# Optimization experiments

Hardware: AMD Instinct MI355X
Metric: run time of the kernel (lower is better)

Reference implementation:

```python
import jax, jax.numpy as jnp
import numpy as np

B, V, H, W, CIN, COUT = 2, 4, 256, 256, 64, 64
WINDOW = 1
GAMMA = 0.1


def setup_inputs() -> dict:
    key = jax.random.key(0)
    ks = jax.random.split(key, 6)
    # gaussian positions: x,y in [-1,1], z in [0.5,2.5] so projection masks are nontrivial
    means = jax.random.uniform(ks[0], (B, V, H, W, 3), dtype=jnp.float32)
    means = means * jnp.array([2.0, 2.0, 2.0], jnp.float32) + jnp.array([-1.0, -1.0, 0.5], jnp.float32)
    depths = jax.random.uniform(ks[1], (B, V, H, W, 1, 1), dtype=jnp.float32)
    gs_feats = jax.random.normal(ks[2], (B, V, H, W, CIN), dtype=jnp.float32)
    # normalized intrinsics (ndc in [0,1))
    intr = jnp.array([[0.8, 0.0, 0.5], [0.0, 0.8, 0.5], [0.0, 0.0, 1.0]], jnp.float32)
    intrinsics = jnp.broadcast_to(intr, (B, V, 3, 3))
    # camera-to-world extrinsics: identity rotation, small per-view translations
    t = jax.random.uniform(ks[3], (B, V, 3), minval=-0.2, maxval=0.2, dtype=jnp.float32)
    extrinsics = jnp.broadcast_to(jnp.eye(4, dtype=jnp.float32), (B, V, 4, 4)).at[..., :3, 3].set(t)
    w1 = jax.random.normal(ks[4], (COUT, CIN, 3, 3), dtype=jnp.float32) * 0.05
    b1 = jnp.zeros((COUT,), jnp.float32)
    w2 = jax.random.normal(ks[5], (COUT, COUT, 3, 3), dtype=jnp.float32) * 0.05
    b2 = jnp.zeros((COUT,), jnp.float32)
    return {"means": means, "depths": depths, "gs_feats": gs_feats,
            "intrinsics": intrinsics, "extrinsics": extrinsics,
            "w1": w1, "b1": b1, "w2": w2, "b2": b2}


def _project(points, intr, extr, eps=1e-8):
    # points (b, n, 3) world; extr (b,4,4) cam-to-world; intr (b,3,3) normalized
    w2c = jnp.linalg.inv(extr)
    ph = jnp.concatenate([points, jnp.ones_like(points[..., :1])], axis=-1)  # (b,n,4)
    cam = jnp.einsum('bij,bnj->bni', w2c, ph)[..., :3]
    z = cam[..., 2:3]
    ndc = jnp.einsum('bij,bnj->bni', intr, cam / (z + eps))
    return ndc[..., :2], cam[..., 2] > eps


def _conv3x3(x, w, b):
    y = jax.lax.conv_general_dilated(x, w, (1, 1), 'SAME',
                                     dimension_numbers=('NCHW', 'OIHW', 'NCHW'))
    return y + b[None, :, None, None]


def reference(means, depths, gs_feats, intrinsics, extrinsics, w1, b1, w2, b2):
    b, v, h, w_, c = gs_feats.shape
    hw = h * w_
    feats_flat = gs_feats.reshape(b, v, hw, c)
    pts = means.reshape(b, v, hw, 3)
    outs = []
    for j in range(v):
        acc = feats_flat[:, j]                      # (b, hw, c)
        norm = jnp.ones((b,), gs_feats.dtype)
        for k in range(v):
            if j != k and (k - WINDOW) <= j <= (k + WINDOW):
                ndc, valid_z = _project(pts[:, j], intrinsics[:, k], extrinsics[:, k])
                px = jnp.floor(ndc[..., 0] * w_).astype(jnp.int32)
                py = jnp.floor(ndc[..., 1] * h).astype(jnp.int32)
                mask = ((ndc[..., 0] >= 0) & (ndc[..., 0] < 1) &
                        (ndc[..., 1] >= 0) & (ndc[..., 1] < 1) & valid_z)  # (b,hw)
                idx = jnp.clip(py, 0, h - 1) * w_ + jnp.clip(px, 0, w_ - 1)
                gathered = jnp.take_along_axis(feats_flat[:, k], idx[..., None], axis=1)
                upd = jnp.where(mask[..., None], gathered, jnp.zeros((), gs_feats.dtype))
                scale = GAMMA * mask.sum(-1).astype(gs_feats.dtype) / (h * w_)  # (b,)
                acc = acc + upd * scale[:, None, None]
                norm = norm + scale
        outs.append(acc / norm[:, None, None])
    fused = jnp.stack(outs, axis=1).reshape(b * v, h, w_, c).transpose(0, 3, 1, 2)  # (bv,c,h,w)
    x = _conv3x3(fused, w1, b1)
    x = jax.nn.gelu(x, approximate=False)
    x = _conv3x3(x, w2, b2)
    return x.transpose(0, 2, 3, 1).reshape(b, v, h, w_, -1)
```

## Files before the change

### kernel.cpp

```cpp
#include <hip/hip_runtime.h>
#include <math.h>

#define HW 65536
#define NPAD 258

typedef short bf16x8 __attribute__((ext_vector_type(8)));
typedef float f32x4  __attribute__((ext_vector_type(4)));

#define O_COUNTS 0
#define O_W2C    2048
#define O_WT     4096
#define O_META   151552
#define O_FUSED  3297280
#define O_X1     71458816

#define HROWB   4224
#define HROWSTR 4240
#define HBUFB   (6 * HROWSTR)

__device__ __forceinline__ unsigned short f2bf(float f) {
    unsigned int u = __float_as_uint(f);
    u += 0x7FFFu + ((u >> 16) & 1u);
    return (unsigned short)(u >> 16);
}

__device__ __forceinline__ unsigned int cvt_pk_bf16(float lo, float hi) {
    unsigned int r;
    asm("v_cvt_pk_bf16_f32 %0, %1, %2" : "=v"(r) : "v"(lo), "v"(hi));
    return r;
}

__device__ __forceinline__ float gelu_fast(float v) {
    float x  = v * 0.70710678118654752f;
    float ax = fabsf(x);
    float t  = __builtin_amdgcn_rcpf(fmaf(0.3275911f, ax, 1.0f));
    float p  = fmaf(t, 1.061405429f, -1.453152027f);
    p = fmaf(t, p, 1.421413741f);
    p = fmaf(t, p, -0.284496736f);
    p = fmaf(t, p, 0.254829592f);
    p = p * t;
    float e   = __expf(-x * x);
    float era = fmaf(-p, e, 1.0f);
    float er  = copysignf(era, x);
    return 0.5f * v * (1.0f + er);
}

__global__ __launch_bounds__(256) void prep_kernel(
    const float* __restrict__ extr, const float* __restrict__ w1,
    const float* __restrict__ w2, float* __restrict__ w2c,
    unsigned short* __restrict__ wT, unsigned short* __restrict__ fusedP,
    unsigned short* __restrict__ x1P, int* __restrict__ counts)
{
    int tid = blockIdx.x * blockDim.x + threadIdx.x;
    int nth = gridDim.x * blockDim.x;

    if (blockIdx.x == 0) {
        if (threadIdx.x < 8) {
            float a[4][8];
            const float* E = extr + threadIdx.x * 16;
            for (int r = 0; r < 4; r++)
                for (int c = 0; c < 4; c++) {
                    a[r][c] = E[r*4 + c];
                    a[r][4+c] = (r == c) ? 1.0f : 0.0f;
                }
            for (int col = 0; col < 4; col++) {
                int piv = col; float bm = fabsf(a[col][col]);
                for (int r = col+1; r < 4; r++) {
                    float v = fabsf(a[r][col]);
                    if (v > bm) { bm = v; piv = r; }
                }
                if (piv != col)
                    for (int c = 0; c < 8; c++) { float t = a[col][c]; a[col][c] = a[piv][c]; a[piv][c] = t; }
                float f = 1.0f / a[col][col];
                for (int c = 0; c < 8; c++) a[col][c] *= f;
                for (int r = 0; r < 4; r++) if (r != col) {
                    float f2 = a[r][col];
                    for (int c = 0; c < 8; c++) a[r][c] -= f2 * a[col][c];
                }
            }
            float* O = w2c + threadIdx.x * 16;
            for (int r = 0; r < 4; r++)
                for (int c = 0; c < 4; c++) O[r*4+c] = a[r][4+c];
        }
    }

    for (int i = tid; i < 384; i += nth) counts[i] = 0;

    for (int e = tid; e < 73728; e += nth) {
        int t = e;
        int j  = t & 7;  t >>= 3;
        int co = t & 63; t >>= 6;
        int q  = t & 3;  t >>= 2;
        int tap = t % 9; t /= 9;
        int h  = t & 1;  int cv = t >> 1;
        int ci = h*32 + q*8 + j;
        int ky = tap / 3, kx = tap % 3;
        const float* wsrc = cv ? w2 : w1;
        float v = wsrc[((co*64 + ci)*3 + ky)*3 + kx];
        wT[cv*36864 + ((((h*9 + tap)*4 + q)*64 + co)*8 + j)] = f2bf(v);
    }

    for (int u = tid; u < 2*8*1028*8; u += nth) {
        int t = u;
        int ch   = t & 7;    t >>= 3;
        int cell = t % 1028; t /= 1028;
        int n    = t & 7;    int buf = t >> 3;
        int y, x;
        if      (cell < 258) { y = 0;   x = cell; }
        else if (cell < 516) { y = 257; x = cell - 258; }
        else if (cell < 772) { y = cell - 516 + 1; x = 0; }
        else                 { y = cell - 772 + 1; x = 257; }
        unsigned short* p = (buf ? x1P : fusedP) +
            (((size_t)(n*NPAD + y)*NPAD + x)*64 + ch*8);
        *reinterpret_cast<uint4*>(p) = make_uint4(0u, 0u, 0u, 0u);
    }
}

__global__ __launch_bounds__(256) void proj_kernel(
    const float* __restrict__ means, const float* __restrict__ intr,
    const float* __restrict__ w2c, int* __restrict__ meta,
    int* __restrict__ counts)
{
    const int jt[6] = {0,1,1,2,2,3};
    const int kt[6] = {1,0,2,1,3,2};
    int s = blockIdx.y;
    int b = s / 6, p = s % 6;
    int j = jt[p], k = kt[p];
    int i = blockIdx.x * 256 + threadIdx.x;

    __shared__ int bcnt;
    if (threadIdx.x == 0) bcnt = 0;
    __syncthreads();

    const float* mp = means + ((size_t)(b*4 + j)*HW + i)*3;
    float x = mp[0], y = mp[1], z = mp[2];
    const float* M = w2c + (b*4 + k)*16;
    const float* I = intr + (b*4 + k)*9;

    float cx = fmaf(M[2],  z, fmaf(M[1], y, M[0]*x)) + M[3];
    float cy = fmaf(M[6],  z, fmaf(M[5], y, M[4]*x)) + M[7];
    float cz = fmaf(M[10], z, fmaf(M[9], y, M[8]*x)) + M[11];

    bool vz = cz > 1e-8f;
    float zi = cz + 1e-8f;
    float sx = cx / zi, sy = cy / zi, sz = cz / zi;
    float nx = fmaf(I[2], sz, fmaf(I[1], sy, I[0]*sx));
    float ny = fmaf(I[5], sz, fmaf(I[4], sy, I[3]*sx));

    int px = (int)floorf(nx * 256.0f);
    int py = (int)floorf(ny * 256.0f);
    bool mask = (nx >= 0.0f) && (nx < 1.0f) && (ny >= 0.0f) && (ny < 1.0f) && vz;
    int pxc = min(max(px, 0), 255);
    int pyc = min(max(py, 0), 255);
    int idx = pyc*256 + pxc;
    meta[(size_t)s*HW + i] = idx | (mask ? (int)0x80000000 : 0);

    unsigned long long bal = __ballot(mask ? 1 : 0);
    if ((threadIdx.x & 63) == 0)
        atomicAdd(&bcnt, (int)__popcll(bal));
    __syncthreads();
    if (threadIdx.x == 0)
        atomicAdd(counts + s*32, bcnt);
}

__global__ __launch_bounds__(256) void fuse_kernel(
    const float* __restrict__ feats, const int* __restrict__ meta,
    const int* __restrict__ counts, unsigned short* __restrict__ fusedP)
{
    const int nsl[4]    = {1, 2, 2, 1};
    const int slt[4][2] = {{0,0},{1,2},{3,4},{5,5}};
    const int kvw[4][2] = {{1,1},{0,2},{1,3},{2,2}};

    int bj = blockIdx.y;
    int b = bj >> 2, j = bj & 3;
    int pt = blockIdx.x * 16 + (threadIdx.x >> 4);
    int cg = threadIdx.x & 15;

    const float4* fj = reinterpret_cast<const float4*>(
        feats + ((size_t)bj*HW + pt)*64) + cg;
    float4 acc = *fj;
    float norm = 1.0f;
    int ns = nsl[j];
    for (int e = 0; e < 2; e++) {
        if (e < ns) {
            int p = slt[j][e], k = kvw[j][e];
            int s = b*6 + p;
            float scale = 0.1f * (float)counts[s*32] / 65536.0f;
            int mt = meta[(size_t)s*HW + pt];
            if (mt < 0) {
                int idx = mt & 0xFFFF;
                const float4* g = reinterpret_cast<const float4*>(
                    feats + ((size_t)(b*4 + k)*HW + idx)*64) + cg;
                float4 gv = *g;
                acc.x += scale * gv.x; acc.y += scale * gv.y;
                acc.z += scale * gv.z; acc.w += scale * gv.w;
            }
            norm += scale;
        }
    }
    float rn = 1.0f / norm;

    int yy = pt >> 8, xx = pt & 255;
    unsigned short* op = fusedP +
        (((size_t)bj*NPAD + (yy+1))*NPAD + (xx+1))*64 + cg*4;
    uint2 o = make_uint2(cvt_pk_bf16(acc.x*rn, acc.y*rn),
                         cvt_pk_bf16(acc.z*rn, acc.w*rn));
    *reinterpret_cast<uint2*>(op) = o;
}

template<int MODE>
__global__ __launch_bounds__(256) void conv_kernel(
    const unsigned short* __restrict__ in, const unsigned short* __restrict__ wT,
    const float* __restrict__ bias, void* __restrict__ outp)
{
    __shared__ unsigned short smem[HBUFB / 2];

    int fid = blockIdx.x;
    int wg  = ((fid & 7) << 8) + (fid >> 3);
    int n   = wg >> 8;
    int rem = wg & 255;
    int y0  = (rem >> 2) << 2;
    int X0  = (rem & 3) << 6;

    int w  = threadIdx.x >> 6;
    int lane = threadIdx.x & 63;
    int m = lane & 15, q = lane >> 4;

    int srcl = ((lane >> 2) * 128) + ((((lane & 3) ^ ((lane >> 3) & 3)) & 3) << 4);
    int tsrcl = 8192 + ((lane >> 2) * 128) + ((lane & 3) << 4);

    int vb[3];
#pragma unroll
    for (int dx = 0; dx < 3; dx++)
        vb[dx] = w*HROWSTR + m*64 + (((q ^ (((m + dx) >> 1) & 3)) & 3) << 4);

    int wvoff = q*1024 + m*16;

    f32x4 acc[4][4];
#pragma unroll
    for (int a = 0; a < 4; a++)
#pragma unroll
        for (int bq = 0; bq < 4; bq++)
            acc[a][bq] = (f32x4){0.f, 0.f, 0.f, 0.f};

#pragma unroll
    for (int h = 0; h < 2; h++) {
        if (h) __syncthreads();

        const char* gb = (const char*)in +
            (((size_t)(n*NPAD) + y0) * NPAD + X0) * 128 + h*64;
        for (int ri = w; ri < 6; ri += 4) {
            const char* g = gb + (size_t)ri * (NPAD*128);
            char* l = (char*)smem + ri*HROWSTR;
#pragma unroll
            for (int i = 0; i < 4; i++)
                __builtin_amdgcn_global_load_lds(
                    (const __attribute__((address_space(1))) unsigned int*)(g + i*2048 + srcl),
                    (__attribute__((address_space(3))) unsigned int*)(l + i*1024 + (size_t)lane*16),
                    16, 0, 0);
            if (lane < 8)
                __builtin_amdgcn_global_load_lds(
                    (const __attribute__((address_space(1))) unsigned int*)(g + tsrcl),
                    (__attribute__((address_space(3))) unsigned int*)(l + 4096 + (size_t)lane*16),
                    16, 0, 0);
        }
        __syncthreads();

        const char* wbase = (const char*)wT + h*36864;
        __builtin_amdgcn_s_setprio(1);
#pragma unroll
        for (int tap = 0; tap < 9; tap++) {
            int dy = tap/3, dx = tap%3;
            const char* wtap = wbase + tap*4096;
            bf16x8 av[4], bv[4];
#pragma unroll
            for (int Mt = 0; Mt < 4; Mt++)
                av[Mt] = *reinterpret_cast<const bf16x8*>(
                    (const char*)smem + vb[dx] + dy*HROWSTR + Mt*1024 + dx*64);
#pragma unroll
            for (int Nt = 0; Nt < 4; Nt++)
                bv[Nt] = *reinterpret_cast<const bf16x8*>(wtap + wvoff + Nt*256);
#pragma unroll
            for (int Mt = 0; Mt < 4; Mt++)
#pragma unroll
                for (int Nt = 0; Nt < 4; Nt++)
                    acc[Mt][Nt] = __builtin_amdgcn_mfma_f32_16x16x32_bf16(
                        bv[Nt], av[Mt], acc[Mt][Nt], 0, 0, 0);
        }
        __builtin_amdgcn_s_setprio(0);
    }

    int yout = y0 + w;
    float4 bsv[4];
#pragma unroll
    for (int Nt = 0; Nt < 4; Nt++)
        bsv[Nt] = *reinterpret_cast<const float4*>(bias + Nt*16 + q*4);

    if (MODE == 1) {
        char* obase = (char*)outp +
            (((size_t)(n*NPAD + yout + 1))*NPAD + (X0 + 1))*128 + m*128 + q*8;
#pragma unroll
        for (int Mt = 0; Mt < 4; Mt++) {
            char* ob = obase + Mt*2048;
#pragma unroll
            for (int Nt = 0; Nt < 4; Nt++) {
                float v0 = gelu_fast(acc[Mt][Nt][0] + bsv[Nt].x);
                float v1 = gelu_fast(acc[Mt][Nt][1] + bsv[Nt].y);
                float v2 = gelu_fast(acc[Mt][Nt][2] + bsv[Nt].z);
                float v3 = gelu_fast(acc[Mt][Nt][3] + bsv[Nt].w);
                uint2 pk = make_uint2(cvt_pk_bf16(v0, v1), cvt_pk_bf16(v2, v3));
                *reinterpret_cast<uint2*>(ob + Nt*32) = pk;
            }
        }
    } else {
        char* obase = (char*)outp +
            (((size_t)(n*256 + yout))*256 + X0)*256 + m*256 + q*16;
#pragma unroll
        for (int Mt = 0; Mt < 4; Mt++) {
            char* ob = obase + Mt*4096;
#pragma unroll
            for (int Nt = 0; Nt < 4; Nt++) {
                float4 v = make_float4(acc[Mt][Nt][0] + bsv[Nt].x,
                                       acc[Mt][Nt][1] + bsv[Nt].y,
                                       acc[Mt][Nt][2] + bsv[Nt].z,
                                       acc[Mt][Nt][3] + bsv[Nt].w);
                *reinterpret_cast<float4*>(ob + Nt*64) = v;
            }
        }
    }
}

extern "C" void kernel_launch(void* const* d_in, const int* in_sizes, int n_in,
                              void* d_out, int out_size, void* d_ws, size_t ws_size,
                              hipStream_t stream)
{
    const float* means = (const float*)d_in[0];
    const float* feats = (const float*)d_in[2];
    const float* intr  = (const float*)d_in[3];
    const float* extr  = (const float*)d_in[4];
    const float* w1    = (const float*)d_in[5];
    const float* b1    = (const float*)d_in[6];
    const float* w2    = (const float*)d_in[7];
    const float* b2    = (const float*)d_in[8];

    char* ws = (char*)d_ws;
    int*            counts = (int*)(ws + O_COUNTS);
    float*          w2c    = (float*)(ws + O_W2C);
    unsigned short* wT     = (unsigned short*)(ws + O_WT);
    int*            meta   = (int*)(ws + O_META);
    unsigned short* fusedP = (unsigned short*)(ws + O_FUSED);
    unsigned short* x1P    = (unsigned short*)(ws + O_X1);

    prep_kernel<<<dim3(96), dim3(256), 0, stream>>>(
        extr, w1, w2, w2c, wT, fusedP, x1P, counts);
    proj_kernel<<<dim3(256, 12), dim3(256), 0, stream>>>(
        means, intr, w2c, meta, counts);
    fuse_kernel<<<dim3(4096, 8), dim3(256), 0, stream>>>(
        feats, meta, counts, fusedP);
    conv_kernel<1><<<dim3(2048), dim3(256), 0, stream>>>(
        fusedP, wT, b1, (void*)x1P);
    conv_kernel<2><<<dim3(2048), dim3(256), 0, stream>>>(
        x1P, wT + 36864, b2, d_out);
}
```

Measured before the change: 388.9 us.

## Double-buffer conv LDS staging and process two row groups per block

The conv kernel now keeps two LDS buffers. It issues the asynchronous global-to-LDS load for the next channel half or row group while MFMA compute runs on the current buffer. Each block handles two 4-row groups, one 128 rows below the other, so the grid is halved. The aim is to hide load latency and cut the block launch and prologue cost. In exchange, LDS use per block roughly doubles, which may lower occupancy and the overlap that came from running several resident blocks.

```diff
diff --git a/kernel.cpp b/kernel.cpp
--- a/kernel.cpp
+++ b/kernel.cpp
@@ -16,7 +16,7 @@
 
 #define HROWB   4224
 #define HROWSTR 4240
-#define HBUFB   (6 * HROWSTR)
+#define HBUF    25440
 
 __device__ __forceinline__ unsigned short f2bf(float f) {
     unsigned int u = __float_as_uint(f);
@@ -213,7 +213,7 @@
     const unsigned short* __restrict__ in, const unsigned short* __restrict__ wT,
     const float* __restrict__ bias, void* __restrict__ outp)
 {
-    __shared__ unsigned short smem[HBUFB / 2];
+    __shared__ unsigned short smem[2 * HBUF / 2];
 
     int fid = blockIdx.x;
     int wg  = ((fid & 7) << 8) + (fid >> 3);
@@ -236,22 +236,15 @@
 
     int wvoff = q*1024 + m*16;
 
-    f32x4 acc[4][4];
-#pragma unroll
-    for (int a = 0; a < 4; a++)
-#pragma unroll
-        for (int bq = 0; bq < 4; bq++)
-            acc[a][bq] = (f32x4){0.f, 0.f, 0.f, 0.f};
-
-#pragma unroll
-    for (int h = 0; h < 2; h++) {
-        if (h) __syncthreads();
-
-        const char* gb = (const char*)in +
-            (((size_t)(n*NPAD) + y0) * NPAD + X0) * 128 + h*64;
+    const char* gb00 = (const char*)in +
+        (((size_t)(n*NPAD) + y0) * NPAD + X0) * 128;
+
+    auto STAGE = [&](int row128, int h, int buf) {
+        const char* gb = gb00 + (size_t)row128 * (NPAD*128) + h*64;
+        char* lb = (char*)smem + buf*HBUF;
         for (int ri = w; ri < 6; ri += 4) {
             const char* g = gb + (size_t)ri * (NPAD*128);
-            char* l = (char*)smem + ri*HROWSTR;
+            char* l = lb + ri*HROWSTR;
 #pragma unroll
             for (int i = 0; i < 4; i++)
                 __builtin_amdgcn_global_load_lds(
@@ -264,8 +257,19 @@
                     (__attribute__((address_space(3))) unsigned int*)(l + 4096 + (size_t)lane*16),
                     16, 0, 0);
         }
-        __syncthreads();
-
+    };
+
+    f32x4 acc[4][4];
+    auto ACCZERO = [&]() {
+#pragma unroll
+        for (int a = 0; a < 4; a++)
+#pragma unroll
+            for (int bq = 0; bq < 4; bq++)
+                acc[a][bq] = (f32x4){0.f, 0.f, 0.f, 0.f};
+    };
+
+    auto COMPUTE = [&](int h, int buf) {
+        const char* sb = (const char*)smem + buf*HBUF;
         const char* wbase = (const char*)wT + h*36864;
         __builtin_amdgcn_s_setprio(1);
 #pragma unroll
@@ -276,7 +280,7 @@
 #pragma unroll
             for (int Mt = 0; Mt < 4; Mt++)
                 av[Mt] = *reinterpret_cast<const bf16x8*>(
-                    (const char*)smem + vb[dx] + dy*HROWSTR + Mt*1024 + dx*64);
+                    sb + vb[dx] + dy*HROWSTR + Mt*1024 + dx*64);
 #pragma unroll
             for (int Nt = 0; Nt < 4; Nt++)
                 bv[Nt] = *reinterpret_cast<const bf16x8*>(wtap + wvoff + Nt*256);
@@ -288,46 +292,68 @@
                         bv[Nt], av[Mt], acc[Mt][Nt], 0, 0, 0);
         }
         __builtin_amdgcn_s_setprio(0);
-    }
-
-    int yout = y0 + w;
-    float4 bsv[4];
-#pragma unroll
-    for (int Nt = 0; Nt < 4; Nt++)
-        bsv[Nt] = *reinterpret_cast<const float4*>(bias + Nt*16 + q*4);
-
-    if (MODE == 1) {
-        char* obase = (char*)outp +
-            (((size_t)(n*NPAD + yout + 1))*NPAD + (X0 + 1))*128 + m*128 + q*8;
-#pragma unroll
-        for (int Mt = 0; Mt < 4; Mt++) {
-            char* ob = obase + Mt*2048;
-#pragma unroll
-            for (int Nt = 0; Nt < 4; Nt++) {
-                float v0 = gelu_fast(acc[Mt][Nt][0] + bsv[Nt].x);
-                float v1 = gelu_fast(acc[Mt][Nt][1] + bsv[Nt].y);
-                float v2 = gelu_fast(acc[Mt][Nt][2] + bsv[Nt].z);
-                float v3 = gelu_fast(acc[Mt][Nt][3] + bsv[Nt].w);
-                uint2 pk = make_uint2(cvt_pk_bf16(v0, v1), cvt_pk_bf16(v2, v3));
-                *reinterpret_cast<uint2*>(ob + Nt*32) = pk;
+    };
+
+    auto EPI = [&](int row128) {
+        int yout = y0 + row128 + w;
+        float4 bsv[4];
+#pragma unroll
+        for (int Nt = 0; Nt < 4; Nt++)
+            bsv[Nt] = *reinterpret_cast<const float4*>(bias + Nt*16 + q*4);
+        if (MODE == 1) {
+            char* obase = (char*)outp +
+                (((size_t)(n*NPAD + yout + 1))*NPAD + (X0 + 1))*128 + m*128 + q*8;
+#pragma unroll
+            for (int Mt = 0; Mt < 4; Mt++) {
+                char* ob = obase + Mt*2048;
+#pragma unroll
+                for (int Nt = 0; Nt < 4; Nt++) {
+                    float v0 = gelu_fast(acc[Mt][Nt][0] + bsv[Nt].x);
+                    float v1 = gelu_fast(acc[Mt][Nt][1] + bsv[Nt].y);
+                    float v2 = gelu_fast(acc[Mt][Nt][2] + bsv[Nt].z);
+                    float v3 = gelu_fast(acc[Mt][Nt][3] + bsv[Nt].w);
+                    uint2 pk = make_uint2(cvt_pk_bf16(v0, v1), cvt_pk_bf16(v2, v3));
+                    *reinterpret_cast<uint2*>(ob + Nt*32) = pk;
+                }
             }
-        }
-    } else {
-        char* obase = (char*)outp +
-            (((size_t)(n*256 + yout))*256 + X0)*256 + m*256 + q*16;
-#pragma unroll
-        for (int Mt = 0; Mt < 4; Mt++) {
-            char* ob = obase + Mt*4096;
-#pragma unroll
-            for (int Nt = 0; Nt < 4; Nt++) {
-                float4 v = make_float4(acc[Mt][Nt][0] + bsv[Nt].x,
-                                       acc[Mt][Nt][1] + bsv[Nt].y,
-                                       acc[Mt][Nt][2] + bsv[Nt].z,
-                                       acc[Mt][Nt][3] + bsv[Nt].w);
-                *reinterpret_cast<float4*>(ob + Nt*64) = v;
+        } else {
+            char* obase = (char*)outp +
+                (((size_t)(n*256 + yout))*256 + X0)*256 + m*256 + q*16;
+#pragma unroll
+            for (int Mt = 0; Mt < 4; Mt++) {
+                char* ob = obase + Mt*4096;
+#pragma unroll
+                for (int Nt = 0; Nt < 4; Nt++) {
+                    float4 v = make_float4(acc[Mt][Nt][0] + bsv[Nt].x,
+                                           acc[Mt][Nt][1] + bsv[Nt].y,
+                                           acc[Mt][Nt][2] + bsv[Nt].z,
+                                           acc[Mt][Nt][3] + bsv[Nt].w);
+                    *reinterpret_cast<float4*>(ob + Nt*64) = v;
+                }
             }
         }
-    }
+    };
+
+    ACCZERO();
+    STAGE(0, 0, 0);
+    __syncthreads();
+
+    STAGE(0, 1, 1);
+    COMPUTE(0, 0);
+    __syncthreads();
+
+    STAGE(128, 0, 0);
+    COMPUTE(1, 1);
+    EPI(0);
+    ACCZERO();
+    __syncthreads();
+
+    STAGE(128, 1, 1);
+    COMPUTE(0, 0);
+    __syncthreads();
+
+    COMPUTE(1, 1);
+    EPI(128);
 }
 
 extern "C" void kernel_launch(void* const* d_in, const int* in_sizes, int n_in,
@@ -357,8 +383,8 @@
         means, intr, w2c, meta, counts);
     fuse_kernel<<<dim3(4096, 8), dim3(256), 0, stream>>>(
         feats, meta, counts, fusedP);
-    conv_kernel<1><<<dim3(2048), dim3(256), 0, stream>>>(
+    conv_kernel<1><<<dim3(1024), dim3(256), 0, stream>>>(
         fusedP, wT, b1, (void*)x1P);
-    conv_kernel<2><<<dim3(2048), dim3(256), 0, stream>>>(
+    conv_kernel<2><<<dim3(1024), dim3(256), 0, stream>>>(
         x1P, wT + 36864, b2, d_out);
 }
```

New measurement: 379.9 us. 2.3% less time.
